# Optimization experiments

Measured on AMD Instinct MI355X. Metric: run time of the kernel, lower is better.

Reference implementation:

```python
import jax, jax.numpy as jnp
import numpy as np
from jax import lax

# problem sizes and solver hyperparameters
B, N, G, T = 8, 128, 100, 24
N_ITERS, LR, RHO = 40, 2e-4, 10.0
VOLL, VOSP = 1000.0, 50.0
RES_UP, RES_DN, RT_UP, RT_DN, RAMP_F = 0.05, 0.02, 2.0, 0.5, 1.0


def setup_inputs() -> dict:
    k = jax.random.split(jax.random.key(0), 8)
    pmin = jax.random.uniform(k[0], (G,), minval=10.0, maxval=50.0)
    pmax = pmin + jax.random.uniform(k[1], (G,), minval=100.0, maxval=300.0)
    b_G = jax.random.uniform(k[2], (G,), minval=10.0, maxval=40.0)
    c_G = jax.random.uniform(k[3], (G,), minval=0.0, maxval=5.0)
    lo, hi = pmin.sum(), pmax.sum()
    forecast = lo + jax.random.uniform(k[4], (B, T)) * 0.5 * (hi - lo)
    omega_scen = 0.05 * hi * jax.random.normal(k[5], (B, N, T))
    om_min = omega_scen.min(axis=1) - 1.0
    om_max = omega_scen.max(axis=1) + 1.0
    eps = jax.random.uniform(k[6], (B,)) * 5.0
    return dict(forecast=forecast, omega_scen=omega_scen, om_min=om_min,
                om_max=om_max, eps=eps, pmin=pmin, pmax=pmax, b_G=b_G, c_G=c_G)


def _solve_one(forecast, omega, om_min, om_max, eps, pmin, pmax, b, c):
    # forecast [T], omega [N,T], om_min/om_max [T], eps scalar
    ramp = pmax * RAMP_F
    rup_p, rdn_p = RES_UP * b, RES_DN * b
    rtu_p, rtd_p = RT_UP * b, RT_DN * b
    dist_max = (om_max[None, :] - omega).sum(-1)   # [N]
    dist_min = (omega - om_min[None, :]).sum(-1)   # [N]

    def objective(v):
        Cost = b[:, None] * v['P'] + c[:, None]
        stage1 = (Cost.sum() + (rup_p[:, None] * v['R_up']).sum()
                  + (rdn_p[:, None] * v['R_dn']).sum())
        Qn = (jnp.einsum('g,ngt->n', rtu_p, v['d_up'])
              + jnp.einsum('g,ngt->n', rtd_p, v['d_dn'])
              + VOLL * v['LS'].sum(-1) + VOSP * v['SP'].sum(-1))
        Qmax = ((rtu_p[:, None] * v['du_max']).sum() + (rtd_p[:, None] * v['dd_max']).sum()
                + VOLL * v['LS_max'].sum() + VOSP * v['SP_max'].sum())
        Qmin = ((rtu_p[:, None] * v['du_min']).sum() + (rtd_p[:, None] * v['dd_min']).sum()
                + VOLL * v['LS_min'].sum() + VOSP * v['SP_min'].sum())
        # epigraph phi[n] >= Qn, >= Qmax - gamma*dist_max, >= Qmin - gamma*dist_min
        phi = jnp.maximum(Qn, jnp.maximum(Qmax - v['gamma'] * dist_max,
                                          Qmin - v['gamma'] * dist_min))
        obj = stage1 + phi.mean() + eps * v['gamma']
        return obj, (phi, Cost)

    def penalty(v):
        relu = jax.nn.relu
        dP = v['P'][:, 1:] - v['P'][:, :-1]
        res = [
            # equality constraints
            v['P'].sum(0) - forecast,
            (v['d_up'] - v['d_dn']).sum(1) + v['LS'] - v['SP'] - omega,
            (v['du_max'] - v['dd_max']).sum(0) + v['LS_max'] - v['SP_max'] - om_max,
            (v['du_min'] - v['dd_min']).sum(0) + v['LS_min'] - v['SP_min'] - om_min,
            # inequality constraints (relu of violation)
            relu(v['P'] + v['R_up'] - pmax[:, None]),
            relu(pmin[:, None] - (v['P'] - v['R_dn'])),
            relu(v['d_up'] - v['R_up'][None]),
            relu(v['d_dn'] - v['R_dn'][None]),
            relu(v['du_max'] - v['R_up']), relu(v['dd_max'] - v['R_dn']),
            relu(v['du_min'] - v['R_up']), relu(v['dd_min'] - v['R_dn']),
            relu(jnp.abs(dP) - ramp[:, None]),
        ]
        total = jnp.zeros(())
        for r in res:
            total = total + (r * r).sum()
        return total

    def loss(v):
        return objective(v)[0] + RHO * penalty(v)

    def project(v):
        v = {kk: jnp.maximum(vv, 0.0) for kk, vv in v.items()}
        v['P'] = jnp.clip(v['P'], pmin[:, None], pmax[:, None])
        return v

    z_gt = jnp.zeros((G, T))
    v0 = {'P': jnp.broadcast_to(0.5 * (pmin + pmax)[:, None], (G, T)),
          'R_up': z_gt, 'R_dn': z_gt,
          'd_up': jnp.zeros((N, G, T)), 'd_dn': jnp.zeros((N, G, T)),
          'LS': jnp.zeros((N, T)), 'SP': jnp.zeros((N, T)),
          'du_max': z_gt, 'dd_max': z_gt,
          'LS_max': jnp.zeros((T,)), 'SP_max': jnp.zeros((T,)),
          'du_min': z_gt, 'dd_min': z_gt,
          'LS_min': jnp.zeros((T,)), 'SP_min': jnp.zeros((T,)),
          'gamma': jnp.zeros(())}
    grad_fn = jax.grad(loss)

    def step(v, _):
        g = grad_fn(v)
        v = jax.tree_util.tree_map(lambda x, gx: x - LR * gx, v, g)
        return project(v), None

    v, _ = lax.scan(step, v0, None, length=N_ITERS)
    obj, (phi, Cost) = objective(v)
    return v['P'], v['R_up'], v['R_dn'], Cost, phi, v['gamma'], obj


def reference(forecast, omega_scen, om_min, om_max, eps, pmin, pmax, b_G, c_G):
    solve = jax.vmap(_solve_one, in_axes=(0, 0, 0, 0, 0, None, None, None, None))
    P, R_up, R_dn, Cost, phi, gamma, obj = solve(
        forecast, omega_scen, om_min, om_max, eps, pmin, pmax, b_G, c_G)
    return P, R_up, R_dn, Cost, phi, gamma, obj
```

## Files before the change

### kernel.cpp

```cpp
#include <hip/hip_runtime.h>
#include <hip/hip_cooperative_groups.h>

namespace cg = cooperative_groups;

#define G_ 100
#define T_ 24
#define NSC 128
#define BATCH 8
#define NITER 40
#define NBLK (BATCH*T_)
#define NTHR 512
#define GMAX 13
#define PAD 32

__device__ __forceinline__ float gload(const float* p){
  return __hip_atomic_load(p, __ATOMIC_RELAXED, __HIP_MEMORY_SCOPE_AGENT);
}
__device__ __forceinline__ void gstore(float* p, float v){
  __hip_atomic_store(p, v, __ATOMIC_RELAXED, __HIP_MEMORY_SCOPE_AGENT);
}
__device__ __forceinline__ unsigned gloadu(const unsigned* p){
  return __hip_atomic_load(p, __ATOMIC_RELAXED, __HIP_MEMORY_SCOPE_AGENT);
}
__device__ __forceinline__ void gstoreu(unsigned* p, unsigned v){
  __hip_atomic_store(p, v, __ATOMIC_RELAXED, __HIP_MEMORY_SCOPE_AGENT);
}

__device__ __forceinline__ void blockReduce2(float& a, float& b, float* sR){
#pragma unroll
  for (int off=32; off; off>>=1){ a+=__shfl_down(a,off,64); b+=__shfl_down(b,off,64); }
  const int w = threadIdx.x>>6;
  __syncthreads();
  if ((threadIdx.x&63)==0){ sR[w]=a; sR[8+w]=b; }
  __syncthreads();
  a=0.f; b=0.f;
#pragma unroll
  for (int i=0;i<8;++i){ a+=sR[i]; b+=sR[8+i]; }
}

__device__ __forceinline__ void waitEpoch(const unsigned* flB, unsigned tgt, int tid, int lane){
  if (tid < 64){
    for (;;){
      unsigned f = (lane < T_) ? gloadu(&flB[lane*PAD]) : tgt;
      if (__ballot(f < tgt) == 0ull) break;
      __builtin_amdgcn_s_sleep(1);
    }
  }
  __syncthreads();
}

__global__ __launch_bounds__(NTHR, 1) void dro_kernel(
    const float* __restrict__ forecast, const float* __restrict__ omega,
    const float* __restrict__ om_min, const float* __restrict__ om_max,
    const float* __restrict__ eps_in, const float* __restrict__ pmin_g,
    const float* __restrict__ pmax_g, const float* __restrict__ bG,
    const float* __restrict__ cG, float* __restrict__ out, float* __restrict__ ws)
{
  constexpr float LR=2e-4f, VOLL=1000.f, VOSP=50.f, TWO_RHO=20.f, INVN=1.f/128.f;
  const int blk=blockIdx.x;
  const int b=blk&7;
  const int t_own=blk>>3;
  const int tid=threadIdx.x, wave=tid>>6, lane=tid&63;
  const int gcnt  = (wave<4)? 13 : 12;
  const int gbase = (wave<4)? wave*13 : 52+(wave-4)*12;

  __shared__ float sRu[G_], sRd[G_];
  __shared__ float sP[G_], sduM[G_], sddM[G_], sdum[G_], sddm[G_];
  __shared__ float sAccU[G_], sAccD[G_];
  __shared__ float sB[G_], sPmin[G_], sPmax[G_], sC[G_];
  __shared__ float sLS[NSC], sSP[NSC], sOm[NSC];
  __shared__ float sGQ[NSC], sR220[NSC];
  __shared__ float sQn[NSC], sDM[NSC], sDm[NSC], sS2[NSC];
  __shared__ float sQp[NSC*9], sSp[NSC*9];
  __shared__ float sQnP[NTHR];
  __shared__ float sRed[40];
  __shared__ float sScal[12];

  float* QNP = ws;
  float* PP  = ws + 73728;
  float* QS  = ws + 147456;
  float* GAM = ws + 165888;
  float* ST1 = ws + 166656;
  unsigned* FLG = (unsigned*)(ws + 172800);

  const float epsv  = eps_in[b];
  const float omaxT = om_max[b*T_ + t_own];
  const float ominT = om_min[b*T_ + t_own];
  const float fctT  = forecast[b*T_ + t_own];
  const unsigned* flB = FLG + b*T_*PAD;
  unsigned* myFlag    = FLG + (b*T_ + t_own)*PAD;

  float duA[GMAX], duB[GMAX], ddA[GMAX], ddB[GMAX];

  if (tid<G_){
    sB[tid]=bG[tid]; sPmin[tid]=pmin_g[tid]; sPmax[tid]=pmax_g[tid]; sC[tid]=cG[tid];
    sRu[tid]=0.f; sRd[tid]=0.f;
    sduM[tid]=0.f; sddM[tid]=0.f; sdum[tid]=0.f; sddm[tid]=0.f;
    sAccU[tid]=0.f; sAccD[tid]=0.f;
  }
  if (tid<NSC){
    const int n=tid;
    sLS[n]=0.f; sSP[n]=0.f; sS2[n]=0.f;
    sOm[n]=omega[(b*NSC+n)*T_+t_own];
    float dM=0.f,dm=0.f;
    for (int t=0;t<T_;++t){
      float o=omega[(b*NSC+n)*T_+t];
      dM+=om_max[b*T_+t]-o; dm+=o-om_min[b*T_+t];
    }
    sDM[n]=dM; sDm[n]=dm;
  }
  if (tid==0){ sScal[3]=0.f; sScal[4]=0.f; sScal[5]=0.f; sScal[6]=0.f; }
  __syncthreads();
#pragma unroll
  for (int j=0;j<GMAX;++j){ duA[j]=0.f; duB[j]=0.f; ddA[j]=0.f; ddB[j]=0.f; }
  {
    float p0=0.f;
    if (tid<G_){
      p0=0.5f*(sPmin[tid]+sPmax[tid]);
      sP[tid]=p0;
      gstore(&PP[b*3072 + t_own*NSC + tid], p0);
    }
    if (tid<NSC) gstore(&QNP[b*3072 + t_own*NSC + tid], 0.f);
    if (tid<2)   gstore(&QS[(b*T_ + t_own)*PAD + tid], 0.f);
    if (t_own==0 && tid==0) gstore(&GAM[b*PAD], 0.f);
    float rp=p0, dum0=0.f;
    blockReduce2(rp,dum0,sRed);
    if (tid==0){
      sScal[0]=-omaxT; sScal[1]=-ominT; sScal[2]=rp-fctT;
      gstoreu(myFlag, 1u);
    }
  }
  __builtin_amdgcn_s_waitcnt(0);
  cg::this_grid().sync();

  for (int k=0;k<=NITER;++k){
    waitEpoch(flB, (unsigned)(k+1), tid, lane);

    const int rb = k%3, wb = (k+1)%3;
    const float* qnpR = QNP + rb*24576 + b*3072;
    const float* ppR  = PP  + rb*24576 + b*3072;
    const float* qsR  = QS  + (rb*BATCH + b)*T_*PAD;
    float* qnpW = QNP + wb*24576 + b*3072 + t_own*NSC;
    float* ppW  = PP  + wb*24576 + b*3072 + t_own*NSC;
    float* qsW  = QS  + (wb*BATCH + b)*T_*PAD + t_own*PAD;

    const float gamma = gload(&GAM[(rb*BATCH + b)*PAD]);
    float pm1=0.f, pp1=0.f;
    if (tid<G_){
      if (t_own>0)     pm1 = gload(&ppR[(t_own-1)*NSC + tid]);
      if (t_own<T_-1)  pp1 = gload(&ppR[(t_own+1)*NSC + tid]);
    }
    {
      const int n = tid&127, sb0 = (tid>>7)*6;
      float q=0.f;
#pragma unroll
      for (int s=0;s<6;++s) q += gload(&qnpR[(sb0+s)*NSC + n]);
      sQnP[tid]=q;
    }
    float Qmax = (tid<T_)? gload(&qsR[tid*PAD])   : 0.f;
    float Qmin = (tid<T_)? gload(&qsR[tid*PAD+1]) : 0.f;

    if (k==NITER){
      blockReduce2(Qmax,Qmin,sRed);
      if (tid<NSC){
        const int n=tid;
        const float qsum=sQnP[n]+sQnP[n+128]+sQnP[n+256]+sQnP[n+384];
        const float m1=Qmax-gamma*sDM[n], m2=Qmin-gamma*sDm[n];
        const float ph=fmaxf(qsum,fmaxf(m1,m2));
        sQn[n]=ph;
        if (t_own==0) out[76800 + b*NSC + n]=ph;
      }
      float st=0.f, dum0=0.f;
      if (tid<G_){
        const int g=tid;
        const float Pv=sP[g];
        const float costv=sB[g]*Pv+sC[g];
        st=costv + 0.05f*sB[g]*sRu[g] + 0.02f*sB[g]*sRd[g];
        const int o=b*2400 + g*T_ + t_own;
        out[o]=Pv;
        out[19200+o]=sRu[g];
        out[38400+o]=sRd[g];
        out[57600+o]=costv;
      }
      blockReduce2(st,dum0,sRed);
      if (tid==0) gstore(&ST1[(b*T_+t_own)*PAD], st);
      if (t_own==0 && tid==0) out[77824+b]=gamma;
      __builtin_amdgcn_s_waitcnt(0);
      __syncthreads();
      if (tid==0) gstoreu(myFlag, (unsigned)(NITER+2));
      if (t_own==0){
        waitEpoch(flB, (unsigned)(NITER+2), tid, lane);
        float pm = (tid<NSC)? sQn[tid] : 0.f;
        float s1 = (tid<T_)? gload(&ST1[(b*T_+tid)*PAD]) : 0.f;
        blockReduce2(pm,s1,sRed);
        if (tid==0) out[77832+b] = s1 + pm*INVN + epsv*gamma;
      }
      break;
    }

    __syncthreads();

    if (wave==0){
#pragma unroll
      for (int off=32; off; off>>=1){ Qmax+=__shfl_xor(Qmax,off,64); Qmin+=__shfl_xor(Qmin,off,64); }
      float g1l=0.f,g2l=0.f,sgl=0.f;
#pragma unroll
      for (int h=0;h<2;++h){
        const int n=lane+h*64;
        const float Qn=sQnP[n]+sQnP[n+128]+sQnP[n+256]+sQnP[n+384];
        const float m1=Qmax-gamma*sDM[n], m2=Qmin-gamma*sDm[n];
        const float inner=fmaxf(m1,m2), ph=fmaxf(Qn,inner);
        const float gQn=(Qn==ph?1.f:0.f)/((inner==ph)?2.f:1.f);
        const float gIn=(inner==ph?1.f:0.f)/((Qn==ph)?2.f:1.f);
        const float gm1=gIn*(m1==inner?1.f:0.f)/((m2==inner)?2.f:1.f);
        const float gm2=gIn*(m2==inner?1.f:0.f)/((m1==inner)?2.f:1.f);
        const float gq=gQn*INVN;
        sGQ[n]=gq;
        g1l+=gm1; g2l+=gm2; sgl+=gm1*sDM[n]+gm2*sDm[n];
        const float r2=sS2[n]+sLS[n]-sSP[n]-sOm[n];
        const float r220=TWO_RHO*r2;
        sR220[n]=r220;
        sLS[n]=fmaxf(sLS[n]-LR*(gq*VOLL+r220),0.f);
        sSP[n]=fmaxf(sSP[n]-LR*(gq*VOSP-r220),0.f);
      }
#pragma unroll
      for (int off=32; off; off>>=1){
        g1l+=__shfl_xor(g1l,off,64); g2l+=__shfl_xor(g2l,off,64); sgl+=__shfl_xor(sgl,off,64);
      }
      if (lane==0){ sScal[8]=g1l; sScal[9]=g2l; sScal[10]=sgl; }
    }
    __syncthreads();

    const float gqA=sGQ[lane],    r220A=sR220[lane];
    const float gqB=sGQ[lane+64], r220B=sR220[lane+64];
    float qvA=0.f,qvB=0.f,svA=0.f,svB=0.f;
#pragma unroll
    for (int j=0;j<GMAX;++j){
      if (j<gcnt){
        const int g=gbase+j;
        const float bg=sB[g];
        const float rtu=2.f*bg, rtd=0.5f*bg;
        const float ru=sRu[g], rd=sRd[g];
        const float r7A=fmaxf(duA[j]-ru,0.f), r8A=fmaxf(ddA[j]-rd,0.f);
        const float r7B=fmaxf(duB[j]-ru,0.f), r8B=fmaxf(ddB[j]-rd,0.f);
        duA[j]=fmaxf(duA[j]-LR*(gqA*rtu+(r220A+TWO_RHO*r7A)),0.f);
        ddA[j]=fmaxf(ddA[j]-LR*(gqA*rtd+(TWO_RHO*r8A-r220A)),0.f);
        duB[j]=fmaxf(duB[j]-LR*(gqB*rtu+(r220B+TWO_RHO*r7B)),0.f);
        ddB[j]=fmaxf(ddB[j]-LR*(gqB*rtd+(TWO_RHO*r8B-r220B)),0.f);
        qvA+=rtu*duA[j]+rtd*ddA[j];  svA+=duA[j]-ddA[j];
        qvB+=rtu*duB[j]+rtd*ddB[j];  svB+=duB[j]-ddB[j];
      }
    }
    sQp[lane*9+wave]=qvA;      sSp[lane*9+wave]=svA;
    sQp[(lane+64)*9+wave]=qvB; sSp[(lane+64)*9+wave]=svB;
    __syncthreads();

    if (tid>=256 && tid<384){
      const int n=tid-256;
      float q=0.f,s=0.f;
#pragma unroll
      for (int w=0;w<8;++w){ q+=sQp[n*9+w]; s+=sSp[n*9+w]; }
      sS2[n]=s;
      q += VOLL*sLS[n]+VOSP*sSP[n];
      gstore(&qnpW[n], q);
    }
    const float r3=sScal[0], r4=sScal[1], rP=sScal[2];
    const float S1s=sScal[8], S2s=sScal[9];
    float pQx=0.f,pQn2=0.f,pr3=0.f,pr4=0.f,pP=0.f;
    if (tid<G_){
      const int g=tid;
      const float rupS=sAccU[g], rdnS=sAccD[g];
      const float Pold=sP[g], ru=sRu[g], rd=sRd[g];
      const float duMo=sduM[g], ddMo=sddM[g], dumo=sdum[g], ddmo=sddm[g];
      const float r5 =fmaxf(Pold+ru-sPmax[g],0.f);
      const float r6 =fmaxf(sPmin[g]-Pold+rd,0.f);
      const float r9 =fmaxf(duMo-ru,0.f), r10=fmaxf(ddMo-rd,0.f);
      const float r11=fmaxf(dumo-ru,0.f), r12=fmaxf(ddmo-rd,0.f);
      const float rampg=sPmax[g];
      float gP=sB[g]+TWO_RHO*(rP+r5-r6);
      if (t_own>0){
        const float dp=Pold-pm1;
        gP+=TWO_RHO*fmaxf(fabsf(dp)-rampg,0.f)*(dp>=0.f?1.f:-1.f);
      }
      if (t_own<T_-1){
        const float dq=pp1-Pold;
        gP-=TWO_RHO*fmaxf(fabsf(dq)-rampg,0.f)*(dq>=0.f?1.f:-1.f);
      }
      const float Pn=fminf(fmaxf(Pold-LR*gP,sPmin[g]),sPmax[g]);
      sP[g]=Pn; gstore(&ppW[g],Pn);
      const float rtuB=2.f*sB[g], rtdB=0.5f*sB[g];
      sRu[g]=fmaxf(ru-LR*(0.05f*sB[g]+TWO_RHO*(r5-rupS-r9-r11)),0.f);
      sRd[g]=fmaxf(rd-LR*(0.02f*sB[g]+TWO_RHO*(r6-rdnS-r10-r12)),0.f);
      const float duMn=fmaxf(duMo-LR*(INVN*S1s*rtuB+TWO_RHO*( r3+r9 )),0.f);
      const float ddMn=fmaxf(ddMo-LR*(INVN*S1s*rtdB+TWO_RHO*(-r3+r10)),0.f);
      const float dumn=fmaxf(dumo-LR*(INVN*S2s*rtuB+TWO_RHO*( r4+r11)),0.f);
      const float ddmn=fmaxf(ddmo-LR*(INVN*S2s*rtdB+TWO_RHO*(-r4+r12)),0.f);
      sduM[g]=duMn; sddM[g]=ddMn; sdum[g]=dumn; sddm[g]=ddmn;
      pQx=rtuB*duMn+rtdB*ddMn; pQn2=rtuB*dumn+rtdB*ddmn;
      pr3=duMn-ddMn; pr4=dumn-ddmn; pP=Pn;
    }
    if (t_own==0 && tid==448)
      gstore(&GAM[(wb*BATCH+b)*PAD], fmaxf(gamma-LR*(epsv-INVN*sScal[10]),0.f));

#pragma unroll
    for (int off=32; off; off>>=1){
      pQx+=__shfl_down(pQx,off,64);  pQn2+=__shfl_down(pQn2,off,64);
      pr3+=__shfl_down(pr3,off,64);  pr4+=__shfl_down(pr4,off,64);
      pP +=__shfl_down(pP,off,64);
    }
    if (lane==0){
      sRed[wave]=pQx; sRed[8+wave]=pQn2; sRed[16+wave]=pr3;
      sRed[24+wave]=pr4; sRed[32+wave]=pP;
    }
    __builtin_amdgcn_s_waitcnt(0);
    __syncthreads();

    if (tid==0){
      float aQx=0.f,aQn2=0.f,a3=0.f,a4=0.f,aP=0.f;
#pragma unroll
      for (int i=0;i<8;++i){
        aQx+=sRed[i]; aQn2+=sRed[8+i]; a3+=sRed[16+i]; a4+=sRed[24+i]; aP+=sRed[32+i];
      }
      const float LSMn=fmaxf(sScal[3]-LR*(INVN*S1s*VOLL+TWO_RHO*r3),0.f);
      const float SPMn=fmaxf(sScal[4]-LR*(INVN*S1s*VOSP-TWO_RHO*r3),0.f);
      const float LSmn=fmaxf(sScal[5]-LR*(INVN*S2s*VOLL+TWO_RHO*r4),0.f);
      const float SPmn=fmaxf(sScal[6]-LR*(INVN*S2s*VOSP-TWO_RHO*r4),0.f);
      sScal[3]=LSMn; sScal[4]=SPMn; sScal[5]=LSmn; sScal[6]=SPmn;
      gstore(&qsW[0], aQx + VOLL*LSMn + VOSP*SPMn);
      gstore(&qsW[1], aQn2 + VOLL*LSmn + VOSP*SPmn);
      sScal[0]=a3 + LSMn - SPMn - omaxT;
      sScal[1]=a4 + LSmn - SPmn - ominT;
      sScal[2]=aP - fctT;
    }
    __builtin_amdgcn_s_waitcnt(0);
    __syncthreads();
    if (tid==0) gstoreu(myFlag, (unsigned)(k+2));

#pragma unroll
    for (int j=0;j<GMAX;++j){
      if (j<gcnt){
        const int g=gbase+j;
        const float ru=sRu[g], rd=sRd[g];
        float aU=fmaxf(duA[j]-ru,0.f)+fmaxf(duB[j]-ru,0.f);
        float aD=fmaxf(ddA[j]-rd,0.f)+fmaxf(ddB[j]-rd,0.f);
#pragma unroll
        for (int off=32; off; off>>=1){ aU+=__shfl_xor(aU,off,64); aD+=__shfl_xor(aD,off,64); }
        if (lane==0){ sAccU[g]=aU; sAccD[g]=aD; }
      }
    }
  }
}

extern "C" void kernel_launch(void* const* d_in, const int* in_sizes, int n_in,
                              void* d_out, int out_size, void* d_ws, size_t ws_size,
                              hipStream_t stream) {
  const float* forecast = (const float*)d_in[0];
  const float* omega    = (const float*)d_in[1];
  const float* omin     = (const float*)d_in[2];
  const float* omax     = (const float*)d_in[3];
  const float* eps      = (const float*)d_in[4];
  const float* pmin     = (const float*)d_in[5];
  const float* pmax     = (const float*)d_in[6];
  const float* bG       = (const float*)d_in[7];
  const float* cG       = (const float*)d_in[8];
  float* out = (float*)d_out;
  float* ws  = (float*)d_ws;
  void* args[] = { &forecast, &omega, &omin, &omax, &eps, &pmin, &pmax, &bG, &cG, &out, &ws };
  hipLaunchCooperativeKernel((const void*)dro_kernel, dim3(NBLK), dim3(NTHR),
                             args, 0, stream);
}
```

Baseline: 498.4 us.

## Replace per-epoch flag barriers with tagged 64-bit value+epoch words

Each value exchanged between blocks is now stored as a 64-bit word holding the float and its iteration tag. Consumers spin only on the specific words they need instead of waiting on per-block epoch flags. This removes the grid sync, the flag writes and the waitcnt/syncthreads that published them, so blocks can proceed as soon as their own inputs arrive. The cost is double the workspace traffic, spinning by many threads, and reliance on 64-bit relaxed atomics being single-copy atomic. The triple-buffer reuse must also stay safe without a global barrier.

```diff
diff --git a/kernel.cpp b/kernel.cpp
--- a/kernel.cpp
+++ b/kernel.cpp
@@ -11,20 +11,20 @@
 #define NBLK (BATCH*T_)
 #define NTHR 512
 #define GMAX 13
-#define PAD 32
-
-__device__ __forceinline__ float gload(const float* p){
+
+typedef unsigned long long u64;
+
+__device__ __forceinline__ u64 gload64(const u64* p){
   return __hip_atomic_load(p, __ATOMIC_RELAXED, __HIP_MEMORY_SCOPE_AGENT);
 }
-__device__ __forceinline__ void gstore(float* p, float v){
+__device__ __forceinline__ void gstore64(u64* p, u64 v){
   __hip_atomic_store(p, v, __ATOMIC_RELAXED, __HIP_MEMORY_SCOPE_AGENT);
 }
-__device__ __forceinline__ unsigned gloadu(const unsigned* p){
-  return __hip_atomic_load(p, __ATOMIC_RELAXED, __HIP_MEMORY_SCOPE_AGENT);
-}
-__device__ __forceinline__ void gstoreu(unsigned* p, unsigned v){
-  __hip_atomic_store(p, v, __ATOMIC_RELAXED, __HIP_MEMORY_SCOPE_AGENT);
-}
+__device__ __forceinline__ u64 pack(float v, unsigned tag){
+  return ((u64)tag<<32) | (u64)__float_as_uint(v);
+}
+__device__ __forceinline__ float unpackv(u64 x){ return __uint_as_float((unsigned)x); }
+__device__ __forceinline__ unsigned unpackt(u64 x){ return (unsigned)(x>>32); }
 
 __device__ __forceinline__ void blockReduce2(float& a, float& b, float* sR){
 #pragma unroll
@@ -36,17 +36,6 @@
   a=0.f; b=0.f;
 #pragma unroll
   for (int i=0;i<8;++i){ a+=sR[i]; b+=sR[8+i]; }
-}
-
-__device__ __forceinline__ void waitEpoch(const unsigned* flB, unsigned tgt, int tid, int lane){
-  if (tid < 64){
-    for (;;){
-      unsigned f = (lane < T_) ? gloadu(&flB[lane*PAD]) : tgt;
-      if (__ballot(f < tgt) == 0ull) break;
-      __builtin_amdgcn_s_sleep(1);
-    }
-  }
-  __syncthreads();
 }
 
 __global__ __launch_bounds__(NTHR, 1) void dro_kernel(
@@ -76,19 +65,17 @@
   __shared__ float sRed[40];
   __shared__ float sScal[12];
 
-  float* QNP = ws;
-  float* PP  = ws + 73728;
-  float* QS  = ws + 147456;
-  float* GAM = ws + 165888;
-  float* ST1 = ws + 166656;
-  unsigned* FLG = (unsigned*)(ws + 172800);
+  u64* W = (u64*)ws;
+  u64* QNP = W;
+  u64* PP  = W + 73728;
+  u64* QS  = W + 147456;
+  u64* GAM = W + 156672;
+  u64* ST1 = W + 157056;
 
   const float epsv  = eps_in[b];
   const float omaxT = om_max[b*T_ + t_own];
   const float ominT = om_min[b*T_ + t_own];
   const float fctT  = forecast[b*T_ + t_own];
-  const unsigned* flB = FLG + b*T_*PAD;
-  unsigned* myFlag    = FLG + (b*T_ + t_own)*PAD;
 
   float duA[GMAX], duB[GMAX], ddA[GMAX], ddB[GMAX];
 
@@ -118,57 +105,86 @@
     if (tid<G_){
       p0=0.5f*(sPmin[tid]+sPmax[tid]);
       sP[tid]=p0;
-      gstore(&PP[b*3072 + t_own*NSC + tid], p0);
-    }
-    if (tid<NSC) gstore(&QNP[b*3072 + t_own*NSC + tid], 0.f);
-    if (tid<2)   gstore(&QS[(b*T_ + t_own)*PAD + tid], 0.f);
-    if (t_own==0 && tid==0) gstore(&GAM[b*PAD], 0.f);
+      gstore64(&PP[b*3072 + t_own*128 + tid], pack(p0,1u));
+    }
+    if (tid<NSC) gstore64(&QNP[b*3072 + t_own*128 + tid], pack(0.f,1u));
+    if (tid<2)   gstore64(&QS[(b*T_ + t_own)*16 + tid], pack(0.f,1u));
+    if (t_own==0 && tid==0) gstore64(&GAM[b*16], pack(0.f,1u));
     float rp=p0, dum0=0.f;
     blockReduce2(rp,dum0,sRed);
     if (tid==0){
       sScal[0]=-omaxT; sScal[1]=-ominT; sScal[2]=rp-fctT;
-      gstoreu(myFlag, 1u);
     }
   }
-  __builtin_amdgcn_s_waitcnt(0);
-  cg::this_grid().sync();
+  __syncthreads();
 
   for (int k=0;k<=NITER;++k){
-    waitEpoch(flB, (unsigned)(k+1), tid, lane);
-
+    const unsigned tg = (unsigned)(k+1);
     const int rb = k%3, wb = (k+1)%3;
-    const float* qnpR = QNP + rb*24576 + b*3072;
-    const float* ppR  = PP  + rb*24576 + b*3072;
-    const float* qsR  = QS  + (rb*BATCH + b)*T_*PAD;
-    float* qnpW = QNP + wb*24576 + b*3072 + t_own*NSC;
-    float* ppW  = PP  + wb*24576 + b*3072 + t_own*NSC;
-    float* qsW  = QS  + (wb*BATCH + b)*T_*PAD + t_own*PAD;
-
-    const float gamma = gload(&GAM[(rb*BATCH + b)*PAD]);
-    float pm1=0.f, pp1=0.f;
+    const u64* qnpR = QNP + rb*24576 + b*3072;
+    const u64* ppR  = PP  + rb*24576 + b*3072;
+    const u64* qsR  = QS  + (rb*BATCH + b)*T_*16;
+    const u64* gamR = GAM + (rb*BATCH + b)*16;
+    u64* qnpW = QNP + wb*24576 + b*3072 + t_own*128;
+    u64* ppW  = PP  + wb*24576 + b*3072 + t_own*128;
+    u64* qsW  = QS  + (wb*BATCH + b)*T_*16 + t_own*16;
+    u64* gamW = GAM + (wb*BATCH + b)*16;
+
+    const int n = tid&127, sb0 = (tid>>7)*6;
+    u64 xq[6];
+#pragma unroll
+    for (int s=0;s<6;++s) xq[s]=gload64(&qnpR[(sb0+s)*128 + n]);
+    u64 xm=0, xp=0;
     if (tid<G_){
-      if (t_own>0)     pm1 = gload(&ppR[(t_own-1)*NSC + tid]);
-      if (t_own<T_-1)  pp1 = gload(&ppR[(t_own+1)*NSC + tid]);
-    }
-    {
-      const int n = tid&127, sb0 = (tid>>7)*6;
-      float q=0.f;
-#pragma unroll
-      for (int s=0;s<6;++s) q += gload(&qnpR[(sb0+s)*NSC + n]);
-      sQnP[tid]=q;
-    }
-    float Qmax = (tid<T_)? gload(&qsR[tid*PAD])   : 0.f;
-    float Qmin = (tid<T_)? gload(&qsR[tid*PAD+1]) : 0.f;
+      if (t_own>0)     xm = gload64(&ppR[(t_own-1)*128 + tid]);
+      if (t_own<T_-1)  xp = gload64(&ppR[(t_own+1)*128 + tid]);
+    }
+    u64 xs0=0, xs1=0, xg=0;
+    if (wave==0){
+      if (lane<T_){ xs0=gload64(&qsR[lane*16]); xs1=gload64(&qsR[lane*16+1]); }
+      xg=gload64(gamR);
+    }
+    for (;;){
+      bool any=false;
+#pragma unroll
+      for (int s=0;s<6;++s)
+        if (unpackt(xq[s])!=tg){ any=true; xq[s]=gload64(&qnpR[(sb0+s)*128 + n]); }
+      if (!any) break;
+      __builtin_amdgcn_s_sleep(1);
+    }
+    if (tid<G_){
+      if (t_own>0)    while (unpackt(xm)!=tg){ __builtin_amdgcn_s_sleep(1); xm=gload64(&ppR[(t_own-1)*128 + tid]); }
+      if (t_own<T_-1) while (unpackt(xp)!=tg){ __builtin_amdgcn_s_sleep(1); xp=gload64(&ppR[(t_own+1)*128 + tid]); }
+    }
+    float Qmax=0.f, Qmin=0.f, gamma=0.f;
+    if (wave==0){
+      if (lane<T_){
+        while (unpackt(xs0)!=tg){ __builtin_amdgcn_s_sleep(1); xs0=gload64(&qsR[lane*16]); }
+        while (unpackt(xs1)!=tg){ __builtin_amdgcn_s_sleep(1); xs1=gload64(&qsR[lane*16+1]); }
+        Qmax=unpackv(xs0); Qmin=unpackv(xs1);
+      }
+      while (unpackt(xg)!=tg){ __builtin_amdgcn_s_sleep(1); xg=gload64(gamR); }
+      gamma=unpackv(xg);
+      if (lane==0) sScal[11]=gamma;
+    }
+    sQnP[tid]=unpackv(xq[0])+unpackv(xq[1])+unpackv(xq[2])
+             +unpackv(xq[3])+unpackv(xq[4])+unpackv(xq[5]);
+    const float pm1=unpackv(xm), pp1=unpackv(xp);
+    __syncthreads();
 
     if (k==NITER){
-      blockReduce2(Qmax,Qmin,sRed);
+      if (wave==0){
+#pragma unroll
+        for (int off=32; off; off>>=1){ Qmax+=__shfl_xor(Qmax,off,64); Qmin+=__shfl_xor(Qmin,off,64); }
+        if (lane==0){ sScal[8]=Qmax; sScal[9]=Qmin; }
+      }
+      __syncthreads();
+      const float Qm=sScal[8], Qn2=sScal[9], gam=sScal[11];
       if (tid<NSC){
-        const int n=tid;
-        const float qsum=sQnP[n]+sQnP[n+128]+sQnP[n+256]+sQnP[n+384];
-        const float m1=Qmax-gamma*sDM[n], m2=Qmin-gamma*sDm[n];
-        const float ph=fmaxf(qsum,fmaxf(m1,m2));
-        sQn[n]=ph;
-        if (t_own==0) out[76800 + b*NSC + n]=ph;
+        const float qsum=sQnP[tid]+sQnP[tid+128]+sQnP[tid+256]+sQnP[tid+384];
+        const float ph=fmaxf(qsum,fmaxf(Qm-gam*sDM[tid],Qn2-gam*sDm[tid]));
+        sQn[tid]=ph;
+        if (t_own==0) out[76800 + b*NSC + tid]=ph;
       }
       float st=0.f, dum0=0.f;
       if (tid<G_){
@@ -183,22 +199,21 @@
         out[57600+o]=costv;
       }
       blockReduce2(st,dum0,sRed);
-      if (tid==0) gstore(&ST1[(b*T_+t_own)*PAD], st);
-      if (t_own==0 && tid==0) out[77824+b]=gamma;
-      __builtin_amdgcn_s_waitcnt(0);
-      __syncthreads();
-      if (tid==0) gstoreu(myFlag, (unsigned)(NITER+2));
+      if (tid==0) gstore64(&ST1[(b*T_+t_own)*16], pack(st,99u));
       if (t_own==0){
-        waitEpoch(flB, (unsigned)(NITER+2), tid, lane);
-        float pm = (tid<NSC)? sQn[tid] : 0.f;
-        float s1 = (tid<T_)? gload(&ST1[(b*T_+tid)*PAD]) : 0.f;
+        if (tid==0) out[77824+b]=gam;
+        float s1=0.f;
+        if (tid<64){
+          u64 xs = (lane<T_)? gload64(&ST1[(b*T_+lane)*16]) : pack(0.f,99u);
+          while (unpackt(xs)!=99u){ __builtin_amdgcn_s_sleep(1); xs=gload64(&ST1[(b*T_+lane)*16]); }
+          s1=unpackv(xs);
+        }
+        float pm=(tid<NSC)? sQn[tid] : 0.f;
         blockReduce2(pm,s1,sRed);
-        if (tid==0) out[77832+b] = s1 + pm*INVN + epsv*gamma;
+        if (tid==0) out[77832+b] = s1 + pm*INVN + epsv*gam;
       }
       break;
     }
-
-    __syncthreads();
 
     if (wave==0){
 #pragma unroll
@@ -206,22 +221,22 @@
       float g1l=0.f,g2l=0.f,sgl=0.f;
 #pragma unroll
       for (int h=0;h<2;++h){
-        const int n=lane+h*64;
-        const float Qn=sQnP[n]+sQnP[n+128]+sQnP[n+256]+sQnP[n+384];
-        const float m1=Qmax-gamma*sDM[n], m2=Qmin-gamma*sDm[n];
+        const int nn=lane+h*64;
+        const float Qn=sQnP[nn]+sQnP[nn+128]+sQnP[nn+256]+sQnP[nn+384];
+        const float m1=Qmax-gamma*sDM[nn], m2=Qmin-gamma*sDm[nn];
         const float inner=fmaxf(m1,m2), ph=fmaxf(Qn,inner);
         const float gQn=(Qn==ph?1.f:0.f)/((inner==ph)?2.f:1.f);
         const float gIn=(inner==ph?1.f:0.f)/((Qn==ph)?2.f:1.f);
         const float gm1=gIn*(m1==inner?1.f:0.f)/((m2==inner)?2.f:1.f);
         const float gm2=gIn*(m2==inner?1.f:0.f)/((m1==inner)?2.f:1.f);
         const float gq=gQn*INVN;
-        sGQ[n]=gq;
-        g1l+=gm1; g2l+=gm2; sgl+=gm1*sDM[n]+gm2*sDm[n];
-        const float r2=sS2[n]+sLS[n]-sSP[n]-sOm[n];
+        sGQ[nn]=gq;
+        g1l+=gm1; g2l+=gm2; sgl+=gm1*sDM[nn]+gm2*sDm[nn];
+        const float r2=sS2[nn]+sLS[nn]-sSP[nn]-sOm[nn];
         const float r220=TWO_RHO*r2;
-        sR220[n]=r220;
-        sLS[n]=fmaxf(sLS[n]-LR*(gq*VOLL+r220),0.f);
-        sSP[n]=fmaxf(sSP[n]-LR*(gq*VOSP-r220),0.f);
+        sR220[nn]=r220;
+        sLS[nn]=fmaxf(sLS[nn]-LR*(gq*VOLL+r220),0.f);
+        sSP[nn]=fmaxf(sSP[nn]-LR*(gq*VOSP-r220),0.f);
       }
 #pragma unroll
       for (int off=32; off; off>>=1){
@@ -255,14 +270,15 @@
     sQp[(lane+64)*9+wave]=qvB; sSp[(lane+64)*9+wave]=svB;
     __syncthreads();
 
+    const unsigned tg2 = (unsigned)(k+2);
     if (tid>=256 && tid<384){
-      const int n=tid-256;
+      const int nn=tid-256;
       float q=0.f,s=0.f;
 #pragma unroll
-      for (int w=0;w<8;++w){ q+=sQp[n*9+w]; s+=sSp[n*9+w]; }
-      sS2[n]=s;
-      q += VOLL*sLS[n]+VOSP*sSP[n];
-      gstore(&qnpW[n], q);
+      for (int w=0;w<8;++w){ q+=sQp[nn*9+w]; s+=sSp[nn*9+w]; }
+      sS2[nn]=s;
+      q += VOLL*sLS[nn]+VOSP*sSP[nn];
+      gstore64(&qnpW[nn], pack(q,tg2));
     }
     const float r3=sScal[0], r4=sScal[1], rP=sScal[2];
     const float S1s=sScal[8], S2s=sScal[9];
@@ -287,7 +303,7 @@
         gP-=TWO_RHO*fmaxf(fabsf(dq)-rampg,0.f)*(dq>=0.f?1.f:-1.f);
       }
       const float Pn=fminf(fmaxf(Pold-LR*gP,sPmin[g]),sPmax[g]);
-      sP[g]=Pn; gstore(&ppW[g],Pn);
+      sP[g]=Pn; gstore64(&ppW[g], pack(Pn,tg2));
       const float rtuB=2.f*sB[g], rtdB=0.5f*sB[g];
       sRu[g]=fmaxf(ru-LR*(0.05f*sB[g]+TWO_RHO*(r5-rupS-r9-r11)),0.f);
       sRd[g]=fmaxf(rd-LR*(0.02f*sB[g]+TWO_RHO*(r6-rdnS-r10-r12)),0.f);
@@ -300,7 +316,7 @@
       pr3=duMn-ddMn; pr4=dumn-ddmn; pP=Pn;
     }
     if (t_own==0 && tid==448)
-      gstore(&GAM[(wb*BATCH+b)*PAD], fmaxf(gamma-LR*(epsv-INVN*sScal[10]),0.f));
+      gstore64(gamW, pack(fmaxf(sScal[11]-LR*(epsv-INVN*sScal[10]),0.f), tg2));
 
 #pragma unroll
     for (int off=32; off; off>>=1){
@@ -312,7 +328,6 @@
       sRed[wave]=pQx; sRed[8+wave]=pQn2; sRed[16+wave]=pr3;
       sRed[24+wave]=pr4; sRed[32+wave]=pP;
     }
-    __builtin_amdgcn_s_waitcnt(0);
     __syncthreads();
 
     if (tid==0){
@@ -326,15 +341,12 @@
       const float LSmn=fmaxf(sScal[5]-LR*(INVN*S2s*VOLL+TWO_RHO*r4),0.f);
       const float SPmn=fmaxf(sScal[6]-LR*(INVN*S2s*VOSP-TWO_RHO*r4),0.f);
       sScal[3]=LSMn; sScal[4]=SPMn; sScal[5]=LSmn; sScal[6]=SPmn;
-      gstore(&qsW[0], aQx + VOLL*LSMn + VOSP*SPMn);
-      gstore(&qsW[1], aQn2 + VOLL*LSmn + VOSP*SPmn);
+      gstore64(&qsW[0], pack(aQx + VOLL*LSMn + VOSP*SPMn, tg2));
+      gstore64(&qsW[1], pack(aQn2 + VOLL*LSmn + VOSP*SPmn, tg2));
       sScal[0]=a3 + LSMn - SPMn - omaxT;
       sScal[1]=a4 + LSmn - SPmn - ominT;
       sScal[2]=aP - fctT;
     }
-    __builtin_amdgcn_s_waitcnt(0);
-    __syncthreads();
-    if (tid==0) gstoreu(myFlag, (unsigned)(k+2));
 
 #pragma unroll
     for (int j=0;j<GMAX;++j){
```

Measured after the change: 476.1 us. 4.5% less time.
